# Optimization experiments

Hardware: AMD Instinct MI355X
Metric: run time of the kernel (lower is better)

## Reference

```python
import jax, jax.numpy as jnp
import numpy as np

B, S, D = 1, 2048, 2048
H, HD = 32, 64  # num_heads, head_dim = hidden_size // num_heads


def setup_inputs() -> dict:
    key = jax.random.key(0)
    ks = jax.random.split(key, 7)
    sc = 0.02
    return {
        "hidden_states": jax.random.normal(ks[0], (B, S, D), dtype=jnp.float32),
        "Wq": jax.random.normal(ks[1], (D, D), dtype=jnp.float32) * sc,
        "Wk": jax.random.normal(ks[2], (D, D), dtype=jnp.float32) * sc,
        "Wv": jax.random.normal(ks[3], (D, D), dtype=jnp.float32) * sc,
        "Wf": jax.random.normal(ks[4], (H, D), dtype=jnp.float32) * sc,
        "bf": jax.random.normal(ks[5], (H,), dtype=jnp.float32),
        "Wo": jax.random.normal(ks[6], (D, D), dtype=jnp.float32) * sc,
    }


def reference(hidden_states, Wq, Wk, Wv, Wf, bf, Wo):
    x = hidden_states
    b, s, _ = x.shape
    # projections (nn.Linear: x @ W^T)
    q = (x @ Wq.T).reshape(b, s, H, HD)
    k = (x @ Wk.T).reshape(b, s, H, HD)
    v = (x @ Wv.T).reshape(b, s, H, HD)
    # per-head log forget gates, computed in float32 as in the torch module
    f = jax.nn.log_sigmoid((x @ Wf.T + bf).astype(jnp.float32))  # [b, s, H]
    # cumulative log decay; FoX bias D_ij = F_i - F_j (sum of log gates over (j, i])
    Fcum = jnp.cumsum(f, axis=1)               # [b, s, H]
    Fh = jnp.transpose(Fcum, (0, 2, 1))        # [b, H, s]
    scale = HD ** -0.5
    scores = jnp.einsum('bqhd,bkhd->bhqk', q, k).astype(jnp.float32) * scale
    scores = scores + Fh[:, :, :, None] - Fh[:, :, None, :]
    causal = jnp.tril(jnp.ones((s, s), dtype=bool))
    scores = jnp.where(causal[None, None], scores, -jnp.inf)
    p = jax.nn.softmax(scores, axis=-1).astype(q.dtype)  # [b, H, q, k]
    o = jnp.einsum('bhqk,bkhd->bqhd', p, v).reshape(b, s, D)
    return o @ Wo.T
```

## Files before the change

kernel.cpp:

```cpp
#include <hip/hip_runtime.h>
#include <stdint.h>

#define SEQ 2048
#define DM  2048
#define NH  32
#define HDIM 64

typedef unsigned short u16;
typedef short bf16x8 __attribute__((ext_vector_type(8)));
typedef float f32x4 __attribute__((ext_vector_type(4)));

__device__ __forceinline__ u16 f2bf(float f) {
    union { float f; uint32_t u; } v; v.f = f;
    uint32_t u = v.u;
    uint32_t r = (u + 0x7fffu + ((u >> 16) & 1u)) >> 16;
    return (u16)r;
}

__global__ __launch_bounds__(256) void convert_bf16(
    const float* __restrict__ X, const float* __restrict__ Wq,
    const float* __restrict__ Wk, const float* __restrict__ Wv,
    const float* __restrict__ Wo,
    u16* __restrict__ Xb, u16* __restrict__ Wqb, u16* __restrict__ Wkb,
    u16* __restrict__ Wvb, u16* __restrict__ Wob)
{
    const int NV = (DM * SEQ) / 4;
    int idx = blockIdx.x * blockDim.x + threadIdx.x;
    int total = NV * 5;
    for (; idx < total; idx += gridDim.x * blockDim.x) {
        int arr = idx / NV, i = idx - arr * NV;
        const float4* s; u16* d;
        switch (arr) {
            case 0:  s = (const float4*)X;  d = Xb;  break;
            case 1:  s = (const float4*)Wq; d = Wqb; break;
            case 2:  s = (const float4*)Wk; d = Wkb; break;
            case 3:  s = (const float4*)Wv; d = Wvb; break;
            default: s = (const float4*)Wo; d = Wob; break;
        }
        float4 v = s[i];
        ushort4 o;
        o.x = f2bf(v.x); o.y = f2bf(v.y); o.z = f2bf(v.z); o.w = f2bf(v.w);
        *(ushort4*)(d + i * 4) = o;
    }
}

__global__ __launch_bounds__(256) void gates_kernel(
    const float* __restrict__ X, const float* __restrict__ Wf,
    const float* __restrict__ bfp, float* __restrict__ F)
{
    int wid = (blockIdx.x * blockDim.x + threadIdx.x) >> 6;
    int lane = threadIdx.x & 63;
    int s = wid >> 5, h = wid & 31;
    const float4* x4 = (const float4*)(X + (size_t)s * DM);
    const float4* w4 = (const float4*)(Wf + (size_t)h * DM);
    float acc = 0.f;
#pragma unroll
    for (int i = 0; i < 8; i++) {
        float4 a = x4[i * 64 + lane], b = w4[i * 64 + lane];
        acc += a.x * b.x + a.y * b.y + a.z * b.z + a.w * b.w;
    }
#pragma unroll
    for (int m = 32; m >= 1; m >>= 1) acc += __shfl_xor(acc, m);
    if (lane == 0) {
        float g = acc + bfp[h];
        float f = fminf(g, 0.f) - log1pf(expf(-fabsf(g)));
        F[h * SEQ + s] = f;
    }
}

__global__ __launch_bounds__(64) void cumsum_kernel(float* __restrict__ F)
{
    int h = blockIdx.x;
    int lane = threadIdx.x;
    float off = 0.f;
    for (int c = 0; c < SEQ / 64; c++) {
        float v = F[h * SEQ + c * 64 + lane];
#pragma unroll
        for (int d = 1; d < 64; d <<= 1) {
            float t = __shfl_up(v, d);
            if (lane >= d) v += t;
        }
        F[h * SEQ + c * 64 + lane] = v + off;
        off += __shfl(v, 63);
    }
}

template <bool STOREF32>
__global__ __launch_bounds__(256) void gemm_bt(
    const u16* __restrict__ A,
    const u16* __restrict__ B0, const u16* __restrict__ B1, const u16* __restrict__ B2,
    void* C0, void* C1, void* C2, int M, int N, int K)
{
    __shared__ u16 lA[128 * 40];
    __shared__ u16 lB[128 * 40];
    int z = blockIdx.z;
    const u16* Bm = (z == 0) ? B0 : ((z == 1) ? B1 : B2);
    void* Cm = (z == 0) ? C0 : ((z == 1) ? C1 : C2);
    int m0 = blockIdx.y * 128, n0 = blockIdx.x * 128;
    int tid = threadIdx.x;
    int wave = tid >> 6, lane = tid & 63, ln = lane & 15, quad = lane >> 4;
    int wr = (wave >> 1) * 64, wc = (wave & 1) * 64;

    f32x4 acc[4][4];
#pragma unroll
    for (int i = 0; i < 4; i++)
#pragma unroll
        for (int j = 0; j < 4; j++)
#pragma unroll
            for (int r = 0; r < 4; r++) acc[i][j][r] = 0.f;

    int srow = tid >> 2, sseg = tid & 3;
    for (int k0 = 0; k0 < K; k0 += 32) {
        __syncthreads();
        *(uint4*)(&lA[srow * 40 + sseg * 8])        = *(const uint4*)(&A[(size_t)(m0 + srow) * K + k0 + sseg * 8]);
        *(uint4*)(&lA[(srow + 64) * 40 + sseg * 8]) = *(const uint4*)(&A[(size_t)(m0 + srow + 64) * K + k0 + sseg * 8]);
        *(uint4*)(&lB[srow * 40 + sseg * 8])        = *(const uint4*)(&Bm[(size_t)(n0 + srow) * K + k0 + sseg * 8]);
        *(uint4*)(&lB[(srow + 64) * 40 + sseg * 8]) = *(const uint4*)(&Bm[(size_t)(n0 + srow + 64) * K + k0 + sseg * 8]);
        __syncthreads();
        bf16x8 af[4], bfr[4];
#pragma unroll
        for (int i = 0; i < 4; i++) af[i]  = *(const bf16x8*)(&lA[(wr + i * 16 + ln) * 40 + quad * 8]);
#pragma unroll
        for (int j = 0; j < 4; j++) bfr[j] = *(const bf16x8*)(&lB[(wc + j * 16 + ln) * 40 + quad * 8]);
#pragma unroll
        for (int i = 0; i < 4; i++)
#pragma unroll
            for (int j = 0; j < 4; j++)
                acc[i][j] = __builtin_amdgcn_mfma_f32_16x16x32_bf16(af[i], bfr[j], acc[i][j], 0, 0, 0);
    }

#pragma unroll
    for (int i = 0; i < 4; i++) {
#pragma unroll
        for (int j = 0; j < 4; j++) {
#pragma unroll
            for (int r = 0; r < 4; r++) {
                int row = m0 + wr + i * 16 + quad * 4 + r;
                int col = n0 + wc + j * 16 + ln;
                float v = acc[i][j][r];
                if (STOREF32) ((float*)Cm)[(size_t)row * N + col] = v;
                else          ((u16*)Cm)[(size_t)row * N + col]   = f2bf(v);
            }
        }
    }
}

__global__ __launch_bounds__(256) void attn_kernel(
    const u16* __restrict__ Q, const u16* __restrict__ K,
    const u16* __restrict__ V, const float* __restrict__ F,
    u16* __restrict__ O)
{
    __shared__ u16 lK[64 * 72];
    __shared__ u16 lV[64 * 72];
    __shared__ u16 lP[4 * 16 * 72];
    __shared__ float lFq[64];
    __shared__ float lFk[64];

    int h = blockIdx.y;
    int q0 = blockIdx.x * 64;
    int tid = threadIdx.x;
    int wave = tid >> 6, lane = tid & 63, ln = lane & 15, quad = lane >> 4;
    const float scale = 0.125f;

    bf16x8 aq[2];
    int qrow = q0 + wave * 16 + ln;
#pragma unroll
    for (int kk = 0; kk < 2; kk++)
        aq[kk] = *(const bf16x8*)(&Q[(size_t)qrow * DM + h * HDIM + kk * 32 + quad * 8]);

    if (tid < 64) lFq[tid] = F[h * SEQ + q0 + tid];

    float m_run[4], l_run[4];
    f32x4 o_acc[4];
#pragma unroll
    for (int r = 0; r < 4; r++) { m_run[r] = -1e30f; l_run[r] = 0.f; }
#pragma unroll
    for (int jo = 0; jo < 4; jo++)
#pragma unroll
        for (int r = 0; r < 4; r++) o_acc[jo][r] = 0.f;

    float Fq0 = F[h * SEQ + q0];
    int nt = q0 / 64 + 1;
    u16* lPw = &lP[wave * 16 * 72];

    for (int kt = 0; kt < nt; kt++) {
        int kb = kt * 64;
        if (kt < nt - 1) {
            float Fkend = F[h * SEQ + kb + 63];
            if (Fq0 - Fkend < -50.f) continue;
        }
        __syncthreads();
        {
            int row = tid >> 3, seg = tid & 7;
            *(uint4*)(&lK[row * 72 + seg * 8])        = *(const uint4*)(&K[(size_t)(kb + row) * DM + h * HDIM + seg * 8]);
            *(uint4*)(&lK[(row + 32) * 72 + seg * 8]) = *(const uint4*)(&K[(size_t)(kb + row + 32) * DM + h * HDIM + seg * 8]);
        }
#pragma unroll
        for (int half = 0; half < 2; half++) {
            int job = half * 256 + tid;
            int kv = job & 63, hs = job >> 6;
            union { uint4 v; u16 e[8]; } tmp;
            tmp.v = *(const uint4*)(&V[(size_t)(kb + kv) * DM + h * HDIM + hs * 8]);
#pragma unroll
            for (int u = 0; u < 8; u++) lV[(hs * 8 + u) * 72 + kv] = tmp.e[u];
        }
        if (tid < 64) lFk[tid] = F[h * SEQ + kb + tid];
        __syncthreads();

        f32x4 s_acc[4];
#pragma unroll
        for (int j = 0; j < 4; j++)
#pragma unroll
            for (int r = 0; r < 4; r++) s_acc[j][r] = 0.f;
#pragma unroll
        for (int kk = 0; kk < 2; kk++)
#pragma unroll
            for (int j = 0; j < 4; j++) {
                bf16x8 bk = *(const bf16x8*)(&lK[(j * 16 + ln) * 72 + kk * 32 + quad * 8]);
                s_acc[j] = __builtin_amdgcn_mfma_f32_16x16x32_bf16(aq[kk], bk, s_acc[j], 0, 0, 0);
            }

        bool diag = (kt == nt - 1);
        int qbase = q0 + wave * 16 + quad * 4;
        float vv[4][4];
        float m_new[4];
#pragma unroll
        for (int r = 0; r < 4; r++) m_new[r] = -1e30f;
#pragma unroll
        for (int j = 0; j < 4; j++) {
            float fk = lFk[j * 16 + ln];
            int kglob = kb + j * 16 + ln;
#pragma unroll
            for (int r = 0; r < 4; r++) {
                float fq = lFq[wave * 16 + quad * 4 + r];
                float v = s_acc[j][r] * scale + (fq - fk);
                if (diag && kglob > qbase + r) v = -1e30f;
                vv[j][r] = v;
                m_new[r] = fmaxf(m_new[r], v);
            }
        }
#pragma unroll
        for (int r = 0; r < 4; r++) {
#pragma unroll
            for (int m = 1; m < 16; m <<= 1) m_new[r] = fmaxf(m_new[r], __shfl_xor(m_new[r], m));
        }
        float alpha[4];
#pragma unroll
        for (int r = 0; r < 4; r++) {
            float mt = fmaxf(m_run[r], m_new[r]);
            alpha[r] = expf(m_run[r] - mt);
            m_run[r] = mt;
        }
        float lsum[4] = {0.f, 0.f, 0.f, 0.f};
#pragma unroll
        for (int j = 0; j < 4; j++)
#pragma unroll
            for (int r = 0; r < 4; r++) {
                float pv = expf(vv[j][r] - m_run[r]);
                vv[j][r] = pv;
                lsum[r] += pv;
            }
#pragma unroll
        for (int r = 0; r < 4; r++) {
#pragma unroll
            for (int m = 1; m < 16; m <<= 1) lsum[r] += __shfl_xor(lsum[r], m);
            l_run[r] = l_run[r] * alpha[r] + lsum[r];
        }
#pragma unroll
        for (int jo = 0; jo < 4; jo++)
#pragma unroll
            for (int r = 0; r < 4; r++) o_acc[jo][r] *= alpha[r];

#pragma unroll
        for (int j = 0; j < 4; j++)
#pragma unroll
            for (int r = 0; r < 4; r++)
                lPw[(quad * 4 + r) * 72 + j * 16 + ln] = f2bf(vv[j][r]);
        __syncthreads();
        bf16x8 ap[2];
#pragma unroll
        for (int kk = 0; kk < 2; kk++)
            ap[kk] = *(const bf16x8*)(&lPw[ln * 72 + kk * 32 + quad * 8]);
#pragma unroll
        for (int kk = 0; kk < 2; kk++)
#pragma unroll
            for (int jo = 0; jo < 4; jo++) {
                bf16x8 bv = *(const bf16x8*)(&lV[(jo * 16 + ln) * 72 + kk * 32 + quad * 8]);
                o_acc[jo] = __builtin_amdgcn_mfma_f32_16x16x32_bf16(ap[kk], bv, o_acc[jo], 0, 0, 0);
            }
    }

#pragma unroll
    for (int r = 0; r < 4; r++) {
        float inv = 1.f / l_run[r];
        int row = q0 + wave * 16 + quad * 4 + r;
#pragma unroll
        for (int jo = 0; jo < 4; jo++)
            O[(size_t)row * DM + h * HDIM + jo * 16 + ln] = f2bf(o_acc[jo][r] * inv);
    }
}

extern "C" void kernel_launch(void* const* d_in, const int* in_sizes, int n_in,
                              void* d_out, int out_size, void* d_ws, size_t ws_size,
                              hipStream_t stream)
{
    const float* X   = (const float*)d_in[0];
    const float* Wq  = (const float*)d_in[1];
    const float* Wk  = (const float*)d_in[2];
    const float* Wv  = (const float*)d_in[3];
    const float* Wf  = (const float*)d_in[4];
    const float* bfp = (const float*)d_in[5];
    const float* Wo  = (const float*)d_in[6];
    float* out = (float*)d_out;

    char* ws = (char*)d_ws;
    const size_t MB8 = (size_t)DM * SEQ * 2;
    u16* Xb  = (u16*)(ws + 0 * MB8);
    u16* Wqb = (u16*)(ws + 1 * MB8);
    u16* Wkb = (u16*)(ws + 2 * MB8);
    u16* Wvb = (u16*)(ws + 3 * MB8);
    u16* Wob = (u16*)(ws + 4 * MB8);
    u16* Qb  = (u16*)(ws + 5 * MB8);
    u16* Kb  = (u16*)(ws + 6 * MB8);
    u16* Vb  = (u16*)(ws + 7 * MB8);
    u16* Ob  = (u16*)(ws + 8 * MB8);
    float* Fb = (float*)(ws + 9 * MB8);

    convert_bf16<<<dim3(4096), dim3(256), 0, stream>>>(X, Wq, Wk, Wv, Wo, Xb, Wqb, Wkb, Wvb, Wob);
    gates_kernel<<<dim3(SEQ * NH / 4), dim3(256), 0, stream>>>(X, Wf, bfp, Fb);
    cumsum_kernel<<<dim3(NH), dim3(64), 0, stream>>>(Fb);
    gemm_bt<false><<<dim3(16, 16, 3), dim3(256), 0, stream>>>(
        Xb, Wqb, Wkb, Wvb, (void*)Qb, (void*)Kb, (void*)Vb, SEQ, DM, DM);
    attn_kernel<<<dim3(SEQ / 64, NH), dim3(256), 0, stream>>>(Qb, Kb, Vb, Fb, Ob);
    gemm_bt<true><<<dim3(16, 16, 1), dim3(256), 0, stream>>>(
        Ob, Wob, Wob, Wob, (void*)out, (void*)out, (void*)out, SEQ, DM, DM);
}
```

Measured before the change: 332.1 us.

## Tile gate projection, parallelize cumsum, use direct global-to-LDS loads in GEMM

The gate projection becomes a shared-memory tiled GEMV with split-K and atomic accumulation, replacing one wave per (seq, head) dot product that reread X for every head. The log-sigmoid and bias move into a cumsum kernel that now scans with 256 threads instead of a serial 64-lane loop. The projection GEMM now loads tiles with global_load_lds straight into unpadded LDS, skipping the register round trip. Risks are LDS bank conflicts from dropping the padding, nondeterministic float atomics in the gate sums, and an added memset.

Result: no change. 333.0 us (+0.3%).

```diff
diff --git a/kernel.cpp b/kernel.cpp
--- a/kernel.cpp
+++ b/kernel.cpp
@@ -16,6 +16,10 @@
     uint32_t r = (u + 0x7fffu + ((u >> 16) & 1u)) >> 16;
     return (u16)r;
 }
+
+#define GLOAD_LDS16(g, l) __builtin_amdgcn_global_load_lds( \
+    (const __attribute__((address_space(1))) uint32_t*)(g), \
+    (__attribute__((address_space(3))) uint32_t*)(l), 16, 0, 0)
 
 __global__ __launch_bounds__(256) void convert_bf16(
     const float* __restrict__ X, const float* __restrict__ Wq,
@@ -46,43 +50,83 @@
 
 __global__ __launch_bounds__(256) void gates_kernel(
     const float* __restrict__ X, const float* __restrict__ Wf,
-    const float* __restrict__ bfp, float* __restrict__ F)
-{
-    int wid = (blockIdx.x * blockDim.x + threadIdx.x) >> 6;
-    int lane = threadIdx.x & 63;
-    int s = wid >> 5, h = wid & 31;
-    const float4* x4 = (const float4*)(X + (size_t)s * DM);
-    const float4* w4 = (const float4*)(Wf + (size_t)h * DM);
-    float acc = 0.f;
+    float* __restrict__ Fraw)
+{
+    __shared__ float lX[64 * 68];
+    __shared__ float lW[32 * 68];
+    int s0 = blockIdx.x * 64;
+    int kp = blockIdx.y;
+    int tid = threadIdx.x;
+    int h = tid & 31, sg = tid >> 5;
+    float acc[8] = {0.f,0.f,0.f,0.f,0.f,0.f,0.f,0.f};
+    for (int k0 = kp * 512; k0 < kp * 512 + 512; k0 += 64) {
+        __syncthreads();
+        {
+            int r = tid >> 2, seg = tid & 3;
+            const float4* src = (const float4*)(X + (size_t)(s0 + r) * DM + k0);
+            float4* dst = (float4*)(&lX[r * 68]);
+#pragma unroll
+            for (int i = 0; i < 4; i++) dst[seg + 4 * i] = src[seg + 4 * i];
+#pragma unroll
+            for (int j = 0; j < 2; j++) {
+                int ii = tid + j * 256;
+                int wr_ = ii >> 4, wc_ = ii & 15;
+                ((float4*)(&lW[wr_ * 68]))[wc_] =
+                    ((const float4*)(Wf + (size_t)wr_ * DM + k0))[wc_];
+            }
+        }
+        __syncthreads();
+#pragma unroll
+        for (int k4 = 0; k4 < 16; k4++) {
+            float4 w = ((const float4*)(&lW[h * 68]))[k4];
+#pragma unroll
+            for (int i = 0; i < 8; i++) {
+                float4 x = ((const float4*)(&lX[(sg + 8 * i) * 68]))[k4];
+                acc[i] += x.x * w.x + x.y * w.y + x.z * w.z + x.w * w.w;
+            }
+        }
+    }
+#pragma unroll
+    for (int i = 0; i < 8; i++)
+        atomicAdd(&Fraw[h * SEQ + s0 + sg + 8 * i], acc[i]);
+}
+
+__global__ __launch_bounds__(256) void cumsum_kernel(
+    float* __restrict__ F, const float* __restrict__ bfp)
+{
+    __shared__ float lws[4];
+    int h = blockIdx.x;
+    int tid = threadIdx.x;
+    int lane = tid & 63, wv = tid >> 6;
+    float bb = bfp[h];
+    float4 a = ((const float4*)(F + (size_t)h * SEQ))[tid * 2];
+    float4 b2 = ((const float4*)(F + (size_t)h * SEQ))[tid * 2 + 1];
+    float v[8] = {a.x, a.y, a.z, a.w, b2.x, b2.y, b2.z, b2.w};
 #pragma unroll
     for (int i = 0; i < 8; i++) {
-        float4 a = x4[i * 64 + lane], b = w4[i * 64 + lane];
-        acc += a.x * b.x + a.y * b.y + a.z * b.z + a.w * b.w;
-    }
-#pragma unroll
-    for (int m = 32; m >= 1; m >>= 1) acc += __shfl_xor(acc, m);
-    if (lane == 0) {
-        float g = acc + bfp[h];
-        float f = fminf(g, 0.f) - log1pf(expf(-fabsf(g)));
-        F[h * SEQ + s] = f;
-    }
-}
-
-__global__ __launch_bounds__(64) void cumsum_kernel(float* __restrict__ F)
-{
-    int h = blockIdx.x;
-    int lane = threadIdx.x;
-    float off = 0.f;
-    for (int c = 0; c < SEQ / 64; c++) {
-        float v = F[h * SEQ + c * 64 + lane];
-#pragma unroll
-        for (int d = 1; d < 64; d <<= 1) {
-            float t = __shfl_up(v, d);
-            if (lane >= d) v += t;
-        }
-        F[h * SEQ + c * 64 + lane] = v + off;
-        off += __shfl(v, 63);
-    }
+        float g = v[i] + bb;
+        v[i] = fminf(g, 0.f) - log1pf(expf(-fabsf(g)));
+    }
+#pragma unroll
+    for (int i = 1; i < 8; i++) v[i] += v[i - 1];
+    float tsum = v[7];
+    float sc = tsum;
+#pragma unroll
+    for (int d = 1; d < 64; d <<= 1) {
+        float t = __shfl_up(sc, d);
+        if (lane >= d) sc += t;
+    }
+    if (lane == 63) lws[wv] = sc;
+    __syncthreads();
+    float woff = 0.f;
+#pragma unroll
+    for (int w2 = 0; w2 < 4; w2++) if (w2 < wv) woff += lws[w2];
+    float off = woff + sc - tsum;
+#pragma unroll
+    for (int i = 0; i < 8; i++) v[i] += off;
+    float4 o1 = {v[0], v[1], v[2], v[3]}, o2 = {v[4], v[5], v[6], v[7]};
+    ((float4*)(F + (size_t)h * SEQ))[tid * 2] = o1;
+    ((float4*)(F + (size_t)h * SEQ))[tid * 2 + 1] = o2;
 }
 
 template <bool STOREF32>
@@ -91,8 +135,8 @@
     const u16* __restrict__ B0, const u16* __restrict__ B1, const u16* __restrict__ B2,
     void* C0, void* C1, void* C2, int M, int N, int K)
 {
-    __shared__ u16 lA[128 * 40];
-    __shared__ u16 lB[128 * 40];
+    __shared__ u16 lA[128 * 32];
+    __shared__ u16 lB[128 * 32];
     int z = blockIdx.z;
     const u16* Bm = (z == 0) ? B0 : ((z == 1) ? B1 : B2);
     void* Cm = (z == 0) ? C0 : ((z == 1) ? C1 : C2);
@@ -109,19 +153,29 @@
 #pragma unroll
             for (int r = 0; r < 4; r++) acc[i][j][r] = 0.f;
 
-    int srow = tid >> 2, sseg = tid & 3;
+    int srow = wave * 32 + (lane >> 2);
+    int scol = (lane & 3) * 8;
+    const u16* gA0 = &A[(size_t)(m0 + srow) * K + scol];
+    const u16* gA1 = &A[(size_t)(m0 + srow + 16) * K + scol];
+    const u16* gB0 = &Bm[(size_t)(n0 + srow) * K + scol];
+    const u16* gB1 = &Bm[(size_t)(n0 + srow + 16) * K + scol];
+    u16* dA0 = &lA[(wave * 32) * 32];
+    u16* dA1 = &lA[(wave * 32 + 16) * 32];
+    u16* dB0 = &lB[(wave * 32) * 32];
+    u16* dB1 = &lB[(wave * 32 + 16) * 32];
+
     for (int k0 = 0; k0 < K; k0 += 32) {
         __syncthreads();
-        *(uint4*)(&lA[srow * 40 + sseg * 8])        = *(const uint4*)(&A[(size_t)(m0 + srow) * K + k0 + sseg * 8]);
-        *(uint4*)(&lA[(srow + 64) * 40 + sseg * 8]) = *(const uint4*)(&A[(size_t)(m0 + srow + 64) * K + k0 + sseg * 8]);
-        *(uint4*)(&lB[srow * 40 + sseg * 8])        = *(const uint4*)(&Bm[(size_t)(n0 + srow) * K + k0 + sseg * 8]);
-        *(uint4*)(&lB[(srow + 64) * 40 + sseg * 8]) = *(const uint4*)(&Bm[(size_t)(n0 + srow + 64) * K + k0 + sseg * 8]);
+        GLOAD_LDS16(gA0 + k0, dA0);
+        GLOAD_LDS16(gA1 + k0, dA1);
+        GLOAD_LDS16(gB0 + k0, dB0);
+        GLOAD_LDS16(gB1 + k0, dB1);
         __syncthreads();
         bf16x8 af[4], bfr[4];
 #pragma unroll
-        for (int i = 0; i < 4; i++) af[i]  = *(const bf16x8*)(&lA[(wr + i * 16 + ln) * 40 + quad * 8]);
-#pragma unroll
-        for (int j = 0; j < 4; j++) bfr[j] = *(const bf16x8*)(&lB[(wc + j * 16 + ln) * 40 + quad * 8]);
+        for (int i = 0; i < 4; i++) af[i]  = *(const bf16x8*)(&lA[(wr + i * 16 + ln) * 32 + quad * 8]);
+#pragma unroll
+        for (int j = 0; j < 4; j++) bfr[j] = *(const bf16x8*)(&lB[(wc + j * 16 + ln) * 32 + quad * 8]);
 #pragma unroll
         for (int i = 0; i < 4; i++)
 #pragma unroll
@@ -326,9 +380,10 @@
     u16* Ob  = (u16*)(ws + 8 * MB8);
     float* Fb = (float*)(ws + 9 * MB8);
 
+    hipMemsetAsync(Fb, 0, (size_t)NH * SEQ * sizeof(float), stream);
     convert_bf16<<<dim3(4096), dim3(256), 0, stream>>>(X, Wq, Wk, Wv, Wo, Xb, Wqb, Wkb, Wvb, Wob);
-    gates_kernel<<<dim3(SEQ * NH / 4), dim3(256), 0, stream>>>(X, Wf, bfp, Fb);
-    cumsum_kernel<<<dim3(NH), dim3(64), 0, stream>>>(Fb);
+    gates_kernel<<<dim3(32, 4), dim3(256), 0, stream>>>(X, Wf, Fb);
+    cumsum_kernel<<<dim3(NH), dim3(256), 0, stream>>>(Fb, bfp);
     gemm_bt<false><<<dim3(16, 16, 3), dim3(256), 0, stream>>>(
         Xb, Wqb, Wkb, Wvb, (void*)Qb, (void*)Kb, (void*)Vb, SEQ, DM, DM);
     attn_kernel<<<dim3(SEQ / 64, NH), dim3(256), 0, stream>>>(Qb, Kb, Vb, Fb, Ob);
```
